# Optimization experiments

Measured on AMD Instinct MI355X. Metric: run time of the kernel, lower is better.

The kernel has to match this reference:

```python
import jax, jax.numpy as jnp
import numpy as np

NUM_ATOM, NUM_CHIRAL = 120, 4
B, N, E = 8, 12500, 80000
D, H = 128, 128  # emb_dim_gnn, hidden_gnn
NEG_SLOPE = 0.2


def setup_inputs() -> dict:
    key = jax.random.key(0)
    ks = jax.random.split(key, 9)
    return {
        "atom_idx": jax.random.randint(ks[0], (B, N), 0, NUM_ATOM, dtype=jnp.int32),
        "chiral_idx": jax.random.randint(ks[1], (B, N), 0, NUM_CHIRAL, dtype=jnp.int32),
        "edge_index": jax.random.randint(ks[2], (B, 2, E), 0, N, dtype=jnp.int32),
        "emb_atom": jax.random.normal(ks[3], (NUM_ATOM, D), jnp.float32) * 0.1,
        "emb_chiral": jax.random.normal(ks[4], (NUM_CHIRAL, D), jnp.float32) * 0.1,
        "W1": jax.random.normal(ks[5], (D, H), jnp.float32) * (1.0 / np.sqrt(D)),
        "b1": jnp.zeros((H,), jnp.float32),
        "W2": jax.random.normal(ks[6], (H, H), jnp.float32) * (1.0 / np.sqrt(H)),
        "b2": jnp.zeros((H,), jnp.float32),
    }


def _gcn_conv(h, src, dst, W, b):
    """PyG GCNConv: linear -> sym-normalized aggregation with self-loops -> bias."""
    n = h.shape[0]
    h = h @ W  # [N, out]
    # degree on destination including self-loop weight 1
    deg = jnp.ones((n,), h.dtype).at[dst].add(1.0)
    dis = jax.lax.rsqrt(deg)  # deg^{-1/2}; deg >= 1 so no inf
    coef = (dis[src] * dis[dst])[:, None]  # [E,1] edge norm
    agg = jnp.zeros_like(h).at[dst].add(h[src] * coef)  # scatter-add messages
    agg = agg + h * (dis * dis)[:, None]  # self-loop contribution norm = deg_i^{-1}
    return agg + b


def _forward_one(atom, chiral, edge, emb_atom, emb_chiral, W1, b1, W2, b2):
    h = emb_atom[atom] + emb_chiral[chiral]  # [N, D]
    src, dst = edge[0], edge[1]
    h = jax.nn.leaky_relu(_gcn_conv(h, src, dst, W1, b1), NEG_SLOPE)
    h = jax.nn.leaky_relu(_gcn_conv(h, src, dst, W2, b2), NEG_SLOPE)
    return h.mean(axis=0)  # graph-level mean pool -> [H]


def reference(atom_idx, chiral_idx, edge_index, emb_atom, emb_chiral, W1, b1, W2, b2):
    f = jax.vmap(_forward_one, in_axes=(0, 0, 0, None, None, None, None, None, None))
    return f(atom_idx, chiral_idx, edge_index, emb_atom, emb_chiral, W1, b1, W2, b2)  # [B, H]
```

## Files before the change

kernel.cpp:

```cpp
#include <hip/hip_runtime.h>
#include <hip/hip_fp16.h>

#define B_ 8
#define N_ 12500
#define E_ 80000
#define D_ 128
#define CAP_ 32

typedef __attribute__((ext_vector_type(8))) short bf16x8;
typedef __attribute__((ext_vector_type(4))) float f32x4;

__device__ inline unsigned short f2bf(float x) {
  unsigned int u = __float_as_uint(x);
  return (unsigned short)((u + 0x7FFFu + ((u >> 16) & 1u)) >> 16);
}
__device__ inline float bflo(unsigned int u) { return __uint_as_float(u << 16); }
__device__ inline float bfhi(unsigned int u) { return __uint_as_float(u & 0xFFFF0000u); }
__device__ inline float h2f(unsigned int hi16) {
  return __half2float(__ushort_as_half((unsigned short)hi16));
}

__global__ __launch_bounds__(256) void k_zero(int* cnt, float* part) {
  int i = blockIdx.x * 256 + threadIdx.x;
  if (i < B_ * N_) cnt[i] = 0;
  if (i < 32 * B_ * D_) part[i] = 0.f;
}

__global__ __launch_bounds__(256) void k_fill_ell(
    const int* __restrict__ edge, const int* __restrict__ atom,
    const int* __restrict__ chiral, int* __restrict__ cnt,
    unsigned int* __restrict__ ellA) {
  int i = blockIdx.x * 256 + threadIdx.x;
  if (i >= B_ * E_) return;
  int b = i / E_, e = i - b * E_;
  const int* eb = edge + (size_t)b * 2 * E_;
  int src = eb[e];
  int dst = eb[E_ + e];
  int comb = atom[b * N_ + src] * 4 + chiral[b * N_ + src];
  int slot = atomicAdd(&cnt[b * N_ + dst], 1);
  if (slot < CAP_)
    ellA[(size_t)(b * N_ + dst) * CAP_ + slot] =
        (unsigned int)src | ((unsigned int)comb << 14);
}

__global__ __launch_bounds__(256) void k_dis(const int* __restrict__ cnt,
                                             float* __restrict__ dis) {
  int i = blockIdx.x * 256 + threadIdx.x;
  if (i < B_ * N_) dis[i] = rsqrtf(1.0f + (float)cnt[i]);
}

__global__ __launch_bounds__(256) void k_coef(const int* __restrict__ cnt,
                                              const float* __restrict__ dis,
                                              unsigned int* __restrict__ ellA,
                                              unsigned int* __restrict__ ellB) {
  int i = blockIdx.x * 256 + threadIdx.x;
  if (i >= B_ * N_ * CAP_) return;
  int row = i >> 5;
  int slot = i & 31;
  int b = row / N_;
  int deg = min(cnt[row], CAP_);
  unsigned int a = 0, bb = 0;
  if (slot < deg) {
    unsigned int t = ellA[i];
    int src = t & 0x3FFF;
    int cmb = t >> 14;
    float coef = dis[b * N_ + src] * dis[row];
    unsigned int cf = (unsigned int)__half_as_ushort(__float2half_rn(coef));
    a = (unsigned int)cmb | (cf << 16);
    bb = (unsigned int)src | (cf << 16);
  }
  ellA[i] = a;
  ellB[i] = bb;
}

__global__ __launch_bounds__(128) void k_tcw(const float* __restrict__ ea,
                                             const float* __restrict__ ec,
                                             const float* __restrict__ W1,
                                             const float* __restrict__ W2,
                                             float* __restrict__ TC,
                                             unsigned short* __restrict__ Wb) {
  int blk = blockIdx.x;
  if (blk < 480) {
    int j = threadIdx.x;
    int a = blk >> 2, c = blk & 3;
    float acc = 0.f;
#pragma unroll 8
    for (int k = 0; k < D_; ++k)
      acc += (ea[a * D_ + k] + ec[c * D_ + k]) * W1[k * D_ + j];
    TC[blk * D_ + j] = acc;
  } else {
    int i = (blk - 480) * 128 + threadIdx.x;
    if (i < D_ * D_) {
      int k = i >> 7, c = i & 127;
      Wb[c * D_ + k] = f2bf(W2[i]);
    }
  }
}

__global__ __launch_bounds__(256) void k_gather1(
    const unsigned int* __restrict__ ellA, const int* __restrict__ cnt,
    const float* __restrict__ dis, const float* __restrict__ TC,
    const int* __restrict__ atom, const int* __restrict__ chiral,
    const float* __restrict__ bias, unsigned short* __restrict__ H1) {
  int b = blockIdx.x & 7;
  int rb = blockIdx.x >> 3;
  int r = rb * 4 + (threadIdx.x >> 6);
  int lane = threadIdx.x & 63;
  int row = __builtin_amdgcn_readfirstlane(b * N_ + r);
  int deg = __builtin_amdgcn_readfirstlane(min(cnt[row], CAP_));
  int base = row * CAP_;
  const float2* TC2 = (const float2*)TC;
  float2 acc = {0.f, 0.f};
  int nb = (deg + 3) >> 2;
  for (int bi = 0; bi < nb; ++bi) {
#pragma unroll
    for (int k = 0; k < 4; ++k) {
      unsigned int t = ellA[base + bi * 4 + k];
      float cj = h2f(t >> 16);
      int cb = (int)(t & 0xFFFFu);
      float2 v = TC2[cb * 64 + lane];
      acc.x += v.x * cj;
      acc.y += v.y * cj;
    }
  }
  int combr = atom[row] * 4 + chiral[row];
  float dr = dis[row];
  float2 h = TC2[combr * 64 + lane];
  float dd = dr * dr;
  float ox = acc.x + h.x * dd + bias[lane * 2 + 0];
  float oy = acc.y + h.y * dd + bias[lane * 2 + 1];
  ox = (ox >= 0.f) ? ox : 0.2f * ox;
  oy = (oy >= 0.f) ? oy : 0.2f * oy;
  unsigned int pk = (unsigned int)f2bf(ox) | ((unsigned int)f2bf(oy) << 16);
  *(unsigned int*)&H1[(size_t)row * D_ + lane * 2] = pk;
}

__global__ __launch_bounds__(256) void k_gemm2(
    const unsigned short* __restrict__ A, const unsigned short* __restrict__ Wb,
    unsigned short* __restrict__ out) {
  int b = blockIdx.x & 7;
  int blk = blockIdx.x >> 3;
  int t = threadIdx.x;
  int wave = t >> 6, lane = t & 63;
  int row0 = blk * 64 + wave * 16;
  int arow = row0 + (lane & 15);
  if (arow >= N_) arow = N_ - 1;
  const unsigned short* Ar = A + ((size_t)b * N_ + arow) * D_;
  int kh = (lane >> 4) * 8;
  bf16x8 af[4];
#pragma unroll
  for (int kc = 0; kc < 4; ++kc) af[kc] = *(const bf16x8*)&Ar[kc * 32 + kh];
  f32x4 acc[8];
#pragma unroll
  for (int ct = 0; ct < 8; ++ct) acc[ct] = (f32x4){0.f, 0.f, 0.f, 0.f};
#pragma unroll
  for (int ct = 0; ct < 8; ++ct) {
    int c = ct * 16 + (lane & 15);
#pragma unroll
    for (int kc = 0; kc < 4; ++kc) {
      bf16x8 bfr = *(const bf16x8*)&Wb[c * D_ + kc * 32 + kh];
      acc[ct] =
          __builtin_amdgcn_mfma_f32_16x16x32_bf16(af[kc], bfr, acc[ct], 0, 0, 0);
    }
  }
  int ro = row0 + (lane >> 4) * 4;
  int co = lane & 15;
#pragma unroll
  for (int ct = 0; ct < 8; ++ct)
#pragma unroll
    for (int rg = 0; rg < 4; ++rg) {
      int r = ro + rg;
      if (r < N_)
        out[((size_t)b * N_ + r) * D_ + ct * 16 + co] = f2bf(acc[ct][rg]);
    }
}

__global__ __launch_bounds__(256) void k_gather2(
    const unsigned int* __restrict__ ellB, const int* __restrict__ cnt,
    const float* __restrict__ dis, const unsigned short* __restrict__ H2,
    const float* __restrict__ bias, float* __restrict__ part) {
  __shared__ float red[4][128];
  int b = blockIdx.x & 7;
  int rb = blockIdx.x >> 3;
  int w = threadIdx.x >> 6;
  int r = rb * 4 + w;
  int lane = threadIdx.x & 63;
  int row = __builtin_amdgcn_readfirstlane(b * N_ + r);
  int deg = __builtin_amdgcn_readfirstlane(min(cnt[row], CAP_));
  int base = row * CAP_;
  const unsigned short* Hb = H2 + (size_t)b * N_ * D_;
  float2 acc = {0.f, 0.f};
  int nb = (deg + 3) >> 2;
  for (int bi = 0; bi < nb; ++bi) {
#pragma unroll
    for (int k = 0; k < 4; ++k) {
      unsigned int t = ellB[base + bi * 4 + k];
      float cj = h2f(t >> 16);
      int s = (int)(t & 0xFFFFu);
      unsigned int u = *(const unsigned int*)&Hb[(size_t)s * D_ + lane * 2];
      acc.x += bflo(u) * cj;
      acc.y += bfhi(u) * cj;
    }
  }
  float dr = dis[row];
  float dd = dr * dr;
  unsigned int uh = *(const unsigned int*)&Hb[(size_t)(row - b * N_) * D_ + lane * 2];
  float ox = acc.x + bflo(uh) * dd + bias[lane * 2 + 0];
  float oy = acc.y + bfhi(uh) * dd + bias[lane * 2 + 1];
  ox = (ox >= 0.f) ? ox : 0.2f * ox;
  oy = (oy >= 0.f) ? oy : 0.2f * oy;
  red[w][lane * 2] = ox;
  red[w][lane * 2 + 1] = oy;
  __syncthreads();
  if (w == 0) {
    float sx = red[0][lane * 2] + red[1][lane * 2] + red[2][lane * 2] +
               red[3][lane * 2];
    float sy = red[0][lane * 2 + 1] + red[1][lane * 2 + 1] +
               red[2][lane * 2 + 1] + red[3][lane * 2 + 1];
    float* pp = part + (size_t)(rb & 31) * (B_ * D_) + b * D_;
    atomicAdd(&pp[lane * 2 + 0], sx);
    atomicAdd(&pp[lane * 2 + 1], sy);
  }
}

__global__ __launch_bounds__(256) void k_outred(const float* __restrict__ part,
                                                float* __restrict__ out) {
  int i = blockIdx.x * 256 + threadIdx.x;
  if (i >= B_ * D_) return;
  float s = 0.f;
#pragma unroll
  for (int p = 0; p < 32; ++p) s += part[p * (B_ * D_) + i];
  out[i] = s * (1.0f / (float)N_);
}

extern "C" void kernel_launch(void* const* d_in, const int* in_sizes, int n_in,
                              void* d_out, int out_size, void* d_ws,
                              size_t ws_size, hipStream_t stream) {
  const int* atom = (const int*)d_in[0];
  const int* chiral = (const int*)d_in[1];
  const int* edge = (const int*)d_in[2];
  const float* emb_atom = (const float*)d_in[3];
  const float* emb_chiral = (const float*)d_in[4];
  const float* W1 = (const float*)d_in[5];
  const float* b1 = (const float*)d_in[6];
  const float* W2 = (const float*)d_in[7];
  const float* b2 = (const float*)d_in[8];
  float* out = (float*)d_out;

  char* w = (char*)d_ws;
  float* dis = (float*)(w + (0ll << 20));
  int* cnt = (int*)(w + (1ll << 20));
  unsigned int* ellA = (unsigned int*)(w + (2ll << 20));
  unsigned int* ellB = (unsigned int*)(w + (16ll << 20));
  float* TC = (float*)(w + (29ll << 20));
  unsigned short* Wb = (unsigned short*)(w + (30ll << 20));
  float* part = (float*)(w + (31ll << 20));
  unsigned short* H1 = (unsigned short*)(w + (32ll << 20));
  unsigned short* H2 = (unsigned short*)(w + (60ll << 20));

  int gBN = (B_ * N_ + 255) / 256;
  int gBE = (B_ * E_ + 255) / 256;
  k_zero<<<gBN, 256, 0, stream>>>(cnt, part);
  k_fill_ell<<<gBE, 256, 0, stream>>>(edge, atom, chiral, cnt, ellA);
  k_dis<<<gBN, 256, 0, stream>>>(cnt, dis);
  k_coef<<<(B_ * N_ * CAP_ + 255) / 256, 256, 0, stream>>>(cnt, dis, ellA,
                                                           ellB);
  k_tcw<<<608, 128, 0, stream>>>(emb_atom, emb_chiral, W1, W2, TC, Wb);

  int gGather = (N_ / 4) * B_;
  int gGemm = ((N_ + 63) / 64) * B_;
  k_gather1<<<gGather, 256, 0, stream>>>(ellA, cnt, dis, TC, atom, chiral, b1,
                                         H1);
  k_gemm2<<<gGemm, 256, 0, stream>>>(H1, Wb, H2);
  k_gather2<<<gGather, 256, 0, stream>>>(ellB, cnt, dis, H2, b2, part);
  k_outred<<<(B_ * D_ + 255) / 256, 256, 0, stream>>>(part, out);
}
```

Measured before the change: 228.9 us.

## Fuse layer-1 gather with layer-2 GEMM through LDS and drop the dis kernel

Layer-1 aggregation now writes its bf16 rows into a shared-memory tile that the MFMA GEMM reads directly, so the H1 round trip through global memory and one launch go away. The separate k_dis kernel is removed and the normalisation is recomputed inline from cnt using rsqrt of the product and 1/(1+deg). The gather loops are unrolled by 8 instead of 4. In exchange each fused block processes 16 rows serially per wave before the GEMM, which lowers gather parallelism and may reduce latency hiding.

```diff
diff --git a/kernel.cpp b/kernel.cpp
--- a/kernel.cpp
+++ b/kernel.cpp
@@ -43,14 +43,7 @@
         (unsigned int)src | ((unsigned int)comb << 14);
 }
 
-__global__ __launch_bounds__(256) void k_dis(const int* __restrict__ cnt,
-                                             float* __restrict__ dis) {
-  int i = blockIdx.x * 256 + threadIdx.x;
-  if (i < B_ * N_) dis[i] = rsqrtf(1.0f + (float)cnt[i]);
-}
-
 __global__ __launch_bounds__(256) void k_coef(const int* __restrict__ cnt,
-                                              const float* __restrict__ dis,
                                               unsigned int* __restrict__ ellA,
                                               unsigned int* __restrict__ ellB) {
   int i = blockIdx.x * 256 + threadIdx.x;
@@ -64,7 +57,8 @@
     unsigned int t = ellA[i];
     int src = t & 0x3FFF;
     int cmb = t >> 14;
-    float coef = dis[b * N_ + src] * dis[row];
+    float coef = rsqrtf((1.0f + (float)cnt[b * N_ + src]) *
+                        (1.0f + (float)cnt[row]));
     unsigned int cf = (unsigned int)__half_as_ushort(__float2half_rn(coef));
     a = (unsigned int)cmb | (cf << 16);
     bb = (unsigned int)src | (cf << 16);
@@ -97,59 +91,56 @@
   }
 }
 
-__global__ __launch_bounds__(256) void k_gather1(
+__global__ __launch_bounds__(256) void k_fused1(
     const unsigned int* __restrict__ ellA, const int* __restrict__ cnt,
-    const float* __restrict__ dis, const float* __restrict__ TC,
-    const int* __restrict__ atom, const int* __restrict__ chiral,
-    const float* __restrict__ bias, unsigned short* __restrict__ H1) {
-  int b = blockIdx.x & 7;
-  int rb = blockIdx.x >> 3;
-  int r = rb * 4 + (threadIdx.x >> 6);
-  int lane = threadIdx.x & 63;
-  int row = __builtin_amdgcn_readfirstlane(b * N_ + r);
-  int deg = __builtin_amdgcn_readfirstlane(min(cnt[row], CAP_));
-  int base = row * CAP_;
-  const float2* TC2 = (const float2*)TC;
-  float2 acc = {0.f, 0.f};
-  int nb = (deg + 3) >> 2;
-  for (int bi = 0; bi < nb; ++bi) {
-#pragma unroll
-    for (int k = 0; k < 4; ++k) {
-      unsigned int t = ellA[base + bi * 4 + k];
-      float cj = h2f(t >> 16);
-      int cb = (int)(t & 0xFFFFu);
-      float2 v = TC2[cb * 64 + lane];
-      acc.x += v.x * cj;
-      acc.y += v.y * cj;
-    }
-  }
-  int combr = atom[row] * 4 + chiral[row];
-  float dr = dis[row];
-  float2 h = TC2[combr * 64 + lane];
-  float dd = dr * dr;
-  float ox = acc.x + h.x * dd + bias[lane * 2 + 0];
-  float oy = acc.y + h.y * dd + bias[lane * 2 + 1];
-  ox = (ox >= 0.f) ? ox : 0.2f * ox;
-  oy = (oy >= 0.f) ? oy : 0.2f * oy;
-  unsigned int pk = (unsigned int)f2bf(ox) | ((unsigned int)f2bf(oy) << 16);
-  *(unsigned int*)&H1[(size_t)row * D_ + lane * 2] = pk;
-}
-
-__global__ __launch_bounds__(256) void k_gemm2(
-    const unsigned short* __restrict__ A, const unsigned short* __restrict__ Wb,
-    unsigned short* __restrict__ out) {
+    const float* __restrict__ TC, const int* __restrict__ atom,
+    const int* __restrict__ chiral, const float* __restrict__ bias,
+    const unsigned short* __restrict__ Wb, unsigned short* __restrict__ out) {
+  __shared__ unsigned short Hs[64][136];
   int b = blockIdx.x & 7;
   int blk = blockIdx.x >> 3;
-  int t = threadIdx.x;
-  int wave = t >> 6, lane = t & 63;
-  int row0 = blk * 64 + wave * 16;
-  int arow = row0 + (lane & 15);
-  if (arow >= N_) arow = N_ - 1;
-  const unsigned short* Ar = A + ((size_t)b * N_ + arow) * D_;
+  int row0 = blk * 64;
+  int wave = threadIdx.x >> 6, lane = threadIdx.x & 63;
+  const float2* TC2 = (const float2*)TC;
+  float bx = bias[lane * 2], by = bias[lane * 2 + 1];
+  for (int rr = 0; rr < 16; ++rr) {
+    int r = row0 + wave * 16 + rr;
+    float ox = 0.f, oy = 0.f;
+    if (r < N_) {
+      int row = __builtin_amdgcn_readfirstlane(b * N_ + r);
+      int cr = __builtin_amdgcn_readfirstlane(cnt[row]);
+      int deg = min(cr, CAP_);
+      int base = row * CAP_;
+      float2 acc = {0.f, 0.f};
+      int nb = (deg + 7) >> 3;
+      for (int bi = 0; bi < nb; ++bi) {
+#pragma unroll
+        for (int k = 0; k < 8; ++k) {
+          unsigned int t = ellA[base + bi * 8 + k];
+          float cj = h2f(t >> 16);
+          int cb = (int)(t & 0xFFFFu);
+          float2 v = TC2[cb * 64 + lane];
+          acc.x += v.x * cj;
+          acc.y += v.y * cj;
+        }
+      }
+      int combr = atom[row] * 4 + chiral[row];
+      float dd = 1.0f / (1.0f + (float)cr);
+      float2 h = TC2[combr * 64 + lane];
+      ox = acc.x + h.x * dd + bx;
+      oy = acc.y + h.y * dd + by;
+      ox = (ox >= 0.f) ? ox : 0.2f * ox;
+      oy = (oy >= 0.f) ? oy : 0.2f * oy;
+    }
+    unsigned int pk = (unsigned int)f2bf(ox) | ((unsigned int)f2bf(oy) << 16);
+    *(unsigned int*)&Hs[wave * 16 + rr][lane * 2] = pk;
+  }
+  int arow = wave * 16 + (lane & 15);
   int kh = (lane >> 4) * 8;
   bf16x8 af[4];
 #pragma unroll
-  for (int kc = 0; kc < 4; ++kc) af[kc] = *(const bf16x8*)&Ar[kc * 32 + kh];
+  for (int kc = 0; kc < 4; ++kc)
+    af[kc] = *(const bf16x8*)&Hs[arow][kc * 32 + kh];
   f32x4 acc[8];
 #pragma unroll
   for (int ct = 0; ct < 8; ++ct) acc[ct] = (f32x4){0.f, 0.f, 0.f, 0.f};
@@ -163,7 +154,7 @@
           __builtin_amdgcn_mfma_f32_16x16x32_bf16(af[kc], bfr, acc[ct], 0, 0, 0);
     }
   }
-  int ro = row0 + (lane >> 4) * 4;
+  int ro = row0 + wave * 16 + (lane >> 4) * 4;
   int co = lane & 15;
 #pragma unroll
   for (int ct = 0; ct < 8; ++ct)
@@ -177,8 +168,8 @@
 
 __global__ __launch_bounds__(256) void k_gather2(
     const unsigned int* __restrict__ ellB, const int* __restrict__ cnt,
-    const float* __restrict__ dis, const unsigned short* __restrict__ H2,
-    const float* __restrict__ bias, float* __restrict__ part) {
+    const unsigned short* __restrict__ H2, const float* __restrict__ bias,
+    float* __restrict__ part) {
   __shared__ float red[4][128];
   int b = blockIdx.x & 7;
   int rb = blockIdx.x >> 3;
@@ -186,15 +177,16 @@
   int r = rb * 4 + w;
   int lane = threadIdx.x & 63;
   int row = __builtin_amdgcn_readfirstlane(b * N_ + r);
-  int deg = __builtin_amdgcn_readfirstlane(min(cnt[row], CAP_));
+  int cr = __builtin_amdgcn_readfirstlane(cnt[row]);
+  int deg = min(cr, CAP_);
   int base = row * CAP_;
   const unsigned short* Hb = H2 + (size_t)b * N_ * D_;
   float2 acc = {0.f, 0.f};
-  int nb = (deg + 3) >> 2;
+  int nb = (deg + 7) >> 3;
   for (int bi = 0; bi < nb; ++bi) {
 #pragma unroll
-    for (int k = 0; k < 4; ++k) {
-      unsigned int t = ellB[base + bi * 4 + k];
+    for (int k = 0; k < 8; ++k) {
+      unsigned int t = ellB[base + bi * 8 + k];
       float cj = h2f(t >> 16);
       int s = (int)(t & 0xFFFFu);
       unsigned int u = *(const unsigned int*)&Hb[(size_t)s * D_ + lane * 2];
@@ -202,9 +194,8 @@
       acc.y += bfhi(u) * cj;
     }
   }
-  float dr = dis[row];
-  float dd = dr * dr;
-  unsigned int uh = *(const unsigned int*)&Hb[(size_t)(row - b * N_) * D_ + lane * 2];
+  float dd = 1.0f / (1.0f + (float)cr);
+  unsigned int uh = *(const unsigned int*)&Hb[(size_t)r * D_ + lane * 2];
   float ox = acc.x + bflo(uh) * dd + bias[lane * 2 + 0];
   float oy = acc.y + bfhi(uh) * dd + bias[lane * 2 + 1];
   ox = (ox >= 0.f) ? ox : 0.2f * ox;
@@ -248,30 +239,25 @@
   float* out = (float*)d_out;
 
   char* w = (char*)d_ws;
-  float* dis = (float*)(w + (0ll << 20));
-  int* cnt = (int*)(w + (1ll << 20));
+  int* cnt = (int*)(w + (0ll << 20));
   unsigned int* ellA = (unsigned int*)(w + (2ll << 20));
   unsigned int* ellB = (unsigned int*)(w + (16ll << 20));
   float* TC = (float*)(w + (29ll << 20));
   unsigned short* Wb = (unsigned short*)(w + (30ll << 20));
   float* part = (float*)(w + (31ll << 20));
-  unsigned short* H1 = (unsigned short*)(w + (32ll << 20));
-  unsigned short* H2 = (unsigned short*)(w + (60ll << 20));
+  unsigned short* H2 = (unsigned short*)(w + (32ll << 20));
 
   int gBN = (B_ * N_ + 255) / 256;
   int gBE = (B_ * E_ + 255) / 256;
   k_zero<<<gBN, 256, 0, stream>>>(cnt, part);
   k_fill_ell<<<gBE, 256, 0, stream>>>(edge, atom, chiral, cnt, ellA);
-  k_dis<<<gBN, 256, 0, stream>>>(cnt, dis);
-  k_coef<<<(B_ * N_ * CAP_ + 255) / 256, 256, 0, stream>>>(cnt, dis, ellA,
-                                                           ellB);
+  k_coef<<<(B_ * N_ * CAP_ + 255) / 256, 256, 0, stream>>>(cnt, ellA, ellB);
   k_tcw<<<608, 128, 0, stream>>>(emb_atom, emb_chiral, W1, W2, TC, Wb);
 
+  int gFused = ((N_ + 63) / 64) * B_;
   int gGather = (N_ / 4) * B_;
-  int gGemm = ((N_ + 63) / 64) * B_;
-  k_gather1<<<gGather, 256, 0, stream>>>(ellA, cnt, dis, TC, atom, chiral, b1,
-                                         H1);
-  k_gemm2<<<gGemm, 256, 0, stream>>>(H1, Wb, H2);
-  k_gather2<<<gGather, 256, 0, stream>>>(ellB, cnt, dis, H2, b2, part);
+  k_fused1<<<gFused, 256, 0, stream>>>(ellA, cnt, TC, atom, chiral, b1, Wb,
+                                       H2);
+  k_gather2<<<gGather, 256, 0, stream>>>(ellB, cnt, H2, b2, part);
   k_outred<<<(B_ * D_ + 255) / 256, 256, 0, stream>>>(part, out);
 }
```

After: 227.8 us. Within noise of the previous version (-0.5%).
